# Kernel optimization log

Hardware: AMD Instinct MI355X
Metric: run time of the kernel (lower is better)

Reference implementation:

```python
import jax, jax.numpy as jnp
import numpy as np

EPS = 1e-8
E, H, F, MCL, V = 256, 512, 100, 500, 128000
CTX = MCL - 1  # encoder facts; decoder appends the mean-fact row
NUM_FACTS = 300


def setup_inputs() -> dict:
    key = jax.random.key(0)
    ks = jax.random.split(key, 16)

    def nrm(k, shape, s=0.02):
        return (jax.random.normal(k, shape) * s).astype(jnp.float32)

    return {
        "context": jax.random.randint(ks[0], (CTX, F), 0, V),
        "word_emb": nrm(ks[1], (V, E)),
        "attn1_W": nrm(ks[2], (MCL, E + H)),
        "attn1_b": nrm(ks[3], (MCL,)),
        "attn2_W": nrm(ks[4], (1, MCL)),
        "attn2_b": nrm(ks[5], (1,)),
        "W_ih": nrm(ks[6], (3 * H, 2 * E + F)),
        "W_hh": nrm(ks[7], (3 * H, H)),
        "b_ih": nrm(ks[8], (3 * H,)),
        "b_hh": nrm(ks[9], (3 * H,)),
        "out1_W": nrm(ks[10], (H, E + H)),
        "out1_b": nrm(ks[11], (H,)),
        "out2_W": nrm(ks[12], (V, H)),
        "out2_b": nrm(ks[13], (V,)),
        "h0": jnp.zeros((1, 1, H), jnp.float32),
        "num_facts": NUM_FACTS,
    }


def _encode(context, word_emb):
    # EncoderModule: embedding lookup + PositionalFactEncoder
    emb = word_emb[context]  # [CTX, F, E]
    s = jnp.arange(F, dtype=jnp.float32) / (F - 1)  # slen axis
    e = jnp.arange(E, dtype=jnp.float32) / (E - 1)  # elen axis
    l = 1.0 - s[:, None] - e[None, :] * (1.0 - 2.0 * s[:, None])  # [F, E]
    return jnp.sum(emb * l[None], axis=1)  # [CTX, E]


def reference(context, word_emb, attn1_W, attn1_b, attn2_W, attn2_b,
              W_ih, W_hh, b_ih, b_hh, out1_W, out1_b, out2_W, out2_b,
              h0, num_facts):
    facts = _encode(context, word_emb)  # [CTX, E]
    mean_fact = jnp.mean(facts[:num_facts], axis=0, keepdims=True)  # [1, E]
    fact_embeddings = jnp.concatenate([facts, mean_fact], axis=0)  # [MCL, E]

    # fact-level attention
    h = jnp.broadcast_to(h0.reshape(1, H), (MCL, H))
    attn_in = jnp.concatenate([fact_embeddings, h], axis=1)  # [MCL, E+H]
    e1 = jnp.tanh(attn_in @ attn1_W.T + attn1_b)  # [MCL, MCL]
    energy = (e1 @ attn2_W.T + attn2_b).reshape(1, -1)  # [1, MCL]
    aw = jax.nn.softmax(energy, axis=1)

    # mask: first num_facts ones, zeros, then 1 for the mean/generate slot
    idx = jnp.arange(MCL)
    mask = jnp.where((idx < num_facts) | (idx == MCL - 1), 1.0, 0.0)[None, :]
    aw = aw * mask + EPS
    aw = aw / jnp.sum(aw)
    log_aw = jnp.log(aw)  # [1, MCL]

    attn_weighted_facts = aw @ fact_embeddings  # [1, E]
    f_max_idx = jnp.argmax(aw, axis=1)[0]
    emb_f_max = fact_embeddings[f_max_idx].reshape(1, E)

    # decoder input: embedding of token 1 + zero positional input
    dec_word = word_emb[1].reshape(1, E)
    dec_pos = jnp.zeros((1, F), jnp.float32)
    x = jnp.concatenate([dec_word, dec_pos, emb_f_max], axis=1)  # [1, 2E+F]

    # torch GRU cell (gates ordered r, z, n)
    hprev = h0.reshape(1, H)
    gi = x @ W_ih.T + b_ih
    gh = hprev @ W_hh.T + b_hh
    r = jax.nn.sigmoid(gi[:, :H] + gh[:, :H])
    z = jax.nn.sigmoid(gi[:, H:2 * H] + gh[:, H:2 * H])
    n = jnp.tanh(gi[:, 2 * H:] + r * gh[:, 2 * H:])
    h_new = (1.0 - z) * n + z * hprev  # [1, H]

    # generate branch (f_t == max_context_len - 1): vocab head
    out = jnp.concatenate([h_new, attn_weighted_facts], axis=1)  # [1, H+E]
    out = jax.nn.relu(out @ out1_W.T + out1_b)
    logits = out @ out2_W.T + out2_b  # [1, V]
    y_pred = jax.nn.log_softmax(logits, axis=1)

    decoder_hidden = h_new.reshape(1, 1, H)
    return y_pred, log_aw, decoder_hidden
```

## Files before the change

### kernel.cpp

```cpp
#include <hip/hip_runtime.h>
#include <math.h>

#define E_    256
#define H_    512
#define F_    100
#define MCL_  500
#define CTX_  499
#define V_    128000
#define EPS_  1e-8f

typedef float f4v __attribute__((ext_vector_type(4)));

#define WS_FE      0
#define WS_ENERGY  (WS_FE + MCL_*E_)
#define WS_EBIAS   (WS_ENERGY + MCL_)
#define WS_AW      (WS_EBIAS + MCL_)
#define WS_AWFP    (WS_AW + 512)
#define WS_FMAX    (WS_AWFP + 8*E_)
#define WS_HNEW    (WS_FMAX + E_)
#define WS_ACT     (WS_HNEW + H_)
#define WS_LOGITS  (WS_ACT + H_)
#define WS_BSUM    (WS_LOGITS + V_)
#define WS_CNT     (WS_BSUM + 1024)

__device__ __forceinline__ float wred64(float v) {
#pragma unroll
  for (int o = 32; o; o >>= 1) v += __shfl_xor(v, o, 64);
  return v;
}
__device__ __forceinline__ float qred16(float v) {
#pragma unroll
  for (int o = 8; o; o >>= 1) v += __shfl_xor(v, o, 64);
  return v;
}
__device__ __forceinline__ float dot4(float4 a, float4 b) {
  return a.x*b.x + a.y*b.y + a.z*b.z + a.w*b.w;
}
__device__ __forceinline__ float dot4v(f4v a, f4v b) {
  return a.x*b.x + a.y*b.y + a.z*b.z + a.w*b.w;
}

__global__ __launch_bounds__(256) void k_encode(const int* __restrict__ ctx,
                                                const float* __restrict__ wemb,
                                                float* __restrict__ fe,
                                                const float* __restrict__ a1W,
                                                const float* __restrict__ a1b,
                                                const float* __restrict__ h0,
                                                float* __restrict__ ebias,
                                                int* __restrict__ cnt) {
  __shared__ int toks[2][F_];
  const int t = threadIdx.x;
  if (blockIdx.x >= 250) {
    const int lane = t & 63, sub = lane & 15, grp = lane >> 4;
    const int wid = (blockIdx.x - 250) * 4 + (t >> 6);
    const float4* h4 = (const float4*)h0;
    float4 hr[8];
#pragma unroll
    for (int q = 0; q < 8; ++q) hr[q] = h4[sub + q * 16];
    for (int j0 = wid * 4; j0 < MCL_; j0 += 32 * 4) {
      const int j = j0 + grp;
      if (j < MCL_) {
        const float4* w4 = (const float4*)(a1W + (size_t)j * (E_ + H_) + E_);
        float acc = 0.f;
#pragma unroll
        for (int q = 0; q < 8; ++q) acc += dot4(w4[sub + q * 16], hr[q]);
        acc = qred16(acc);
        if (sub == 0) ebias[j] = acc + a1b[j];
      }
    }
    return;
  }
  if (blockIdx.x == 0 && t == 0) *cnt = 0;
  const int i0 = blockIdx.x * 2;
  const int i1 = i0 + 1;
  if (t < F_) toks[0][t] = ctx[i0 * F_ + t];
  else if (t < 2 * F_) toks[1][t - F_] = (i1 < CTX_) ? ctx[i1 * F_ + (t - F_)] : 0;
  __syncthreads();
  const int row = t >> 7, tt = t & 127;
  const int i = i0 + row;
  const float e0n = (2 * tt) * (1.0f / 255.0f);
  const float e1n = (2 * tt + 1) * (1.0f / 255.0f);
  float ax = 0.f, ay = 0.f, bx = 0.f, by = 0.f;
#pragma unroll
  for (int f0 = 0; f0 < F_; f0 += 10) {
    float2 vb[10];
#pragma unroll
    for (int u = 0; u < 10; ++u)
      vb[u] = ((const float2*)(wemb + (size_t)toks[row][f0 + u] * E_))[tt];
#pragma unroll
    for (int u = 0; u < 10; ++u) {
      float s = (f0 + u) * (1.0f / 99.0f);
      float A = 1.0f - s, B = 1.0f - 2.0f * s;
      if (u & 1) { bx = fmaf(vb[u].x, A - e0n * B, bx); by = fmaf(vb[u].y, A - e1n * B, by); }
      else       { ax = fmaf(vb[u].x, A - e0n * B, ax); ay = fmaf(vb[u].y, A - e1n * B, ay); }
    }
  }
  if (i < CTX_) {
    float2 r; r.x = ax + bx; r.y = ay + by;
    ((float2*)(fe + (size_t)i * E_))[tt] = r;
  }
}

__global__ __launch_bounds__(256) void k_energy(float* __restrict__ fe,
                                                const float* __restrict__ a1W,
                                                const float* __restrict__ ebias,
                                                const float* __restrict__ a2W,
                                                const float* __restrict__ a2b,
                                                const int* __restrict__ nfp,
                                                float* __restrict__ energy,
                                                float* __restrict__ aw_ws,
                                                float* __restrict__ fmaxrow,
                                                float* __restrict__ out_logaw,
                                                int* __restrict__ cnt) {
  __shared__ float sfe[4][E_];
  __shared__ float sred[4][256];
  __shared__ int sticket;
  const int t = threadIdx.x;
  const int i0 = blockIdx.x * 4;
  const int nf = *nfp;

  if (blockIdx.x == 124) {
    float s0 = 0.f, s1 = 0.f, s2 = 0.f, s3 = 0.f;
    float s4 = 0.f, s5 = 0.f, s6 = 0.f, s7 = 0.f;
    int i = 0;
    for (; i + 8 <= nf; i += 8) {
      s0 += fe[(i + 0) * E_ + t]; s1 += fe[(i + 1) * E_ + t];
      s2 += fe[(i + 2) * E_ + t]; s3 += fe[(i + 3) * E_ + t];
      s4 += fe[(i + 4) * E_ + t]; s5 += fe[(i + 5) * E_ + t];
      s6 += fe[(i + 6) * E_ + t]; s7 += fe[(i + 7) * E_ + t];
    }
    for (; i < nf; ++i) s0 += fe[i * E_ + t];
    float mv = (((s0 + s1) + (s2 + s3)) + ((s4 + s5) + (s6 + s7))) / (float)nf;
    sfe[3][t] = mv;
    fe[CTX_ * E_ + t] = mv;
    sfe[0][t] = fe[496 * E_ + t];
    sfe[1][t] = fe[497 * E_ + t];
    sfe[2][t] = fe[498 * E_ + t];
  } else {
#pragma unroll
    for (int r = 0; r < 4; ++r) sfe[r][t] = fe[(i0 + r) * E_ + t];
  }
  __syncthreads();
  float c0 = 0.f, c1 = 0.f, c2 = 0.f, c3 = 0.f;
  const float4* s0p = (const float4*)sfe[0];
  const float4* s1p = (const float4*)sfe[1];
  const float4* s2p = (const float4*)sfe[2];
  const float4* s3p = (const float4*)sfe[3];
  for (int j = t; j < MCL_; j += 256) {
    const float4* w4 = (const float4*)(a1W + (size_t)j * (E_ + H_));
    float d0 = 0.f, d1 = 0.f, d2 = 0.f, d3 = 0.f;
#pragma unroll 8
    for (int q = 0; q < E_ / 4; ++q) {
      float4 a = w4[q];
      d0 += dot4(a, s0p[q]);
      d1 += dot4(a, s1p[q]);
      d2 += dot4(a, s2p[q]);
      d3 += dot4(a, s3p[q]);
    }
    float bj = ebias[j], wj = a2W[j];
    c0 = fmaf(wj, tanhf(d0 + bj), c0);
    c1 = fmaf(wj, tanhf(d1 + bj), c1);
    c2 = fmaf(wj, tanhf(d2 + bj), c2);
    c3 = fmaf(wj, tanhf(d3 + bj), c3);
  }
  sred[0][t] = c0; sred[1][t] = c1; sred[2][t] = c2; sred[3][t] = c3;
  __syncthreads();
  for (int s = 128; s; s >>= 1) {
    if (t < s) {
#pragma unroll
      for (int r = 0; r < 4; ++r) sred[r][t] += sred[r][t + s];
    }
    __syncthreads();
  }
  if (t < 4) energy[i0 + t] = sred[t][0] + a2b[0];

  __threadfence();
  if (t == 0) sticket = atomicAdd(cnt, 1);
  __syncthreads();
  if (sticket != 124) return;
  __threadfence();

  float* red = sred[0];
  int* idx = (int*)sred[1];
  float ev0 = energy[t];
  float ev1 = (t + 256 < MCL_) ? energy[t + 256] : -1e30f;
  red[t] = fmaxf(ev0, ev1); __syncthreads();
  for (int s = 128; s; s >>= 1) { if (t < s) red[t] = fmaxf(red[t], red[t + s]); __syncthreads(); }
  const float mx = red[0]; __syncthreads();

  float p0 = __expf(ev0 - mx);
  float p1 = (t + 256 < MCL_) ? __expf(ev1 - mx) : 0.f;
  red[t] = p0 + p1; __syncthreads();
  for (int s = 128; s; s >>= 1) { if (t < s) red[t] += red[t + s]; __syncthreads(); }
  const float S1 = red[0]; __syncthreads();

  float m0 = ((t < nf) || (t == MCL_ - 1)) ? 1.f : 0.f;
  float m1 = (((t + 256) < nf) || ((t + 256) == MCL_ - 1)) ? 1.f : 0.f;
  float a0 = p0 / S1 * m0 + EPS_;
  float a1 = (t + 256 < MCL_) ? (p1 / S1 * m1 + EPS_) : 0.f;
  red[t] = a0 + a1; __syncthreads();
  for (int s = 128; s; s >>= 1) { if (t < s) red[t] += red[t + s]; __syncthreads(); }
  const float S2 = red[0]; __syncthreads();

  a0 /= S2; a1 /= S2;
  out_logaw[t] = logf(a0);
  aw_ws[t] = a0;
  if (t + 256 < MCL_) { out_logaw[t + 256] = logf(a1); aw_ws[t + 256] = a1; }

  float bv; int bi;
  if ((t + 256 < MCL_) && (a1 > a0)) { bv = a1; bi = t + 256; } else { bv = a0; bi = t; }
  red[t] = bv; idx[t] = bi; __syncthreads();
  for (int s = 128; s; s >>= 1) {
    if (t < s) {
      float o = red[t + s]; int oi = idx[t + s];
      if (o > red[t] || (o == red[t] && oi < idx[t])) { red[t] = o; idx[t] = oi; }
    }
    __syncthreads();
  }
  const int fidx = idx[0]; __syncthreads();
  fmaxrow[t] = fe[fidx * E_ + t];
}

__global__ __launch_bounds__(256) void k_gates_gru(const float* __restrict__ Wih,
                                                   const float* __restrict__ bih,
                                                   const float* __restrict__ Whh,
                                                   const float* __restrict__ bhh,
                                                   const float* __restrict__ wemb,
                                                   const float* __restrict__ fmaxrow,
                                                   const float* __restrict__ h0,
                                                   const float* __restrict__ aw,
                                                   const float* __restrict__ fe,
                                                   float* __restrict__ awfp,
                                                   float* __restrict__ hnew,
                                                   float* __restrict__ out_hidden) {
  const int t = threadIdx.x;
  const int b = blockIdx.x;
  if (b >= 128) {
    const int m = b - 128;
    const int lo = m * 63;
    const int hi = min(MCL_, lo + 63);
    float pa = 0.f, pb = 0.f, pc = 0.f, pd = 0.f;
    int i = lo;
    for (; i + 4 <= hi; i += 4) {
      pa = fmaf(aw[i], fe[i * E_ + t], pa);
      pb = fmaf(aw[i + 1], fe[(i + 1) * E_ + t], pb);
      pc = fmaf(aw[i + 2], fe[(i + 2) * E_ + t], pc);
      pd = fmaf(aw[i + 3], fe[(i + 3) * E_ + t], pd);
    }
    for (; i < hi; ++i) pa = fmaf(aw[i], fe[i * E_ + t], pa);
    awfp[m * E_ + t] = (pa + pb) + (pc + pd);
    return;
  }
  const int lane = t & 63, w = t >> 6;
  const int h = b * 4 + w;
  const float4* xa4 = (const float4*)(wemb + E_);
  const float4* xb4 = (const float4*)fmaxrow;
  const float4* h4  = (const float4*)h0;
  float4 xav = xa4[lane], xbv = xb4[lane];
  float4 hva = h4[lane], hvb = h4[lane + 64];
  const float* rr = Wih + (size_t)h * (2 * E_ + F_);
  const float* rz = Wih + (size_t)(H_ + h) * (2 * E_ + F_);
  const float* rn = Wih + (size_t)(2 * H_ + h) * (2 * E_ + F_);
  float gir = dot4(((const float4*)rr)[lane], xav) + dot4(((const float4*)(rr + E_ + F_))[lane], xbv);
  float giz = dot4(((const float4*)rz)[lane], xav) + dot4(((const float4*)(rz + E_ + F_))[lane], xbv);
  float gin = dot4(((const float4*)rn)[lane], xav) + dot4(((const float4*)(rn + E_ + F_))[lane], xbv);
  const float4* wr = (const float4*)(Whh + (size_t)h * H_);
  const float4* wz = (const float4*)(Whh + (size_t)(H_ + h) * H_);
  const float4* wn = (const float4*)(Whh + (size_t)(2 * H_ + h) * H_);
  float ghr = dot4(wr[lane], hva) + dot4(wr[lane + 64], hvb);
  float ghz = dot4(wz[lane], hva) + dot4(wz[lane + 64], hvb);
  float ghn = dot4(wn[lane], hva) + dot4(wn[lane + 64], hvb);
  gir = wred64(gir); giz = wred64(giz); gin = wred64(gin);
  ghr = wred64(ghr); ghz = wred64(ghz); ghn = wred64(ghn);
  if (lane == 0) {
    float r = 1.f / (1.f + __expf(-(gir + bih[h] + ghr + bhh[h])));
    float z = 1.f / (1.f + __expf(-(giz + bih[H_ + h] + ghz + bhh[H_ + h])));
    float n = tanhf(gin + bih[2 * H_ + h] + r * (ghn + bhh[2 * H_ + h]));
    float hv = (1.f - z) * n + z * h0[h];
    hnew[h] = hv;
    out_hidden[h] = hv;
  }
}

__global__ __launch_bounds__(256) void k_out1(const float* __restrict__ o1W,
                                              const float* __restrict__ o1b,
                                              const float* __restrict__ hnew,
                                              const float* __restrict__ awfp,
                                              float* __restrict__ act) {
  __shared__ float cat[H_ + E_];
  const int t = threadIdx.x;
#pragma unroll
  for (int idx = t; idx < H_; idx += 256) cat[idx] = hnew[idx];
  {
    float s = 0.f;
#pragma unroll
    for (int q = 0; q < 8; ++q) s += awfp[q * E_ + t];
    cat[H_ + t] = s;
  }
  __syncthreads();
  const int lane = t & 63, w = t >> 6;
  const int r = blockIdx.x * 4 + w;
  const float4* c4 = (const float4*)cat;
  const float4* w4 = (const float4*)(o1W + (size_t)r * (H_ + E_));
  float acc = 0.f;
#pragma unroll
  for (int q = 0; q < 3; ++q) acc += dot4(w4[lane + 64 * q], c4[lane + 64 * q]);
  acc = wred64(acc);
  if (lane == 0) act[r] = fmaxf(acc + o1b[r], 0.f);
}

__global__ __launch_bounds__(256) void k_vocab(const float* __restrict__ o2W,
                                               const float* __restrict__ o2b,
                                               const float* __restrict__ act,
                                               float* __restrict__ logits,
                                               float* __restrict__ bsum) {
  __shared__ float swsum[4];
  const int t = threadIdx.x;
  const int lane = t & 63, sub = lane & 15, grp = lane >> 4, w = t >> 6;
  const int gw = blockIdx.x * 4 + w;
  const int nW = 1024 * 4;
  const f4v* a4 = (const f4v*)act;
  f4v ar[8];
#pragma unroll
  for (int q = 0; q < 8; ++q) ar[q] = a4[sub + q * 16];
  float sumexp = 0.f;
  for (int v0 = gw * 8; v0 < V_; v0 += nW * 8) {
    const int vA = v0 + grp;
    const int vB = v0 + 4 + grp;
    float accA = 0.f, accB = 0.f;
    if (vB < V_) {
      const f4v* wa = (const f4v*)(o2W + (size_t)vA * H_);
      const f4v* wb = (const f4v*)(o2W + (size_t)vB * H_);
      f4v la[8], lb[8];
#pragma unroll
      for (int q = 0; q < 8; ++q) la[q] = __builtin_nontemporal_load(&wa[sub + q * 16]);
#pragma unroll
      for (int q = 0; q < 8; ++q) lb[q] = __builtin_nontemporal_load(&wb[sub + q * 16]);
#pragma unroll
      for (int q = 0; q < 8; ++q) { accA += dot4v(la[q], ar[q]); accB += dot4v(lb[q], ar[q]); }
    } else if (vA < V_) {
      const f4v* wa = (const f4v*)(o2W + (size_t)vA * H_);
      f4v la[8];
#pragma unroll
      for (int q = 0; q < 8; ++q) la[q] = __builtin_nontemporal_load(&wa[sub + q * 16]);
#pragma unroll
      for (int q = 0; q < 8; ++q) accA += dot4v(la[q], ar[q]);
    }
    accA = qred16(accA);
    accB = qred16(accB);
    if (sub == 0) {
      if (vA < V_) { float lg = accA + o2b[vA]; logits[vA] = lg; sumexp += __expf(lg); }
      if (vB < V_) { float lg = accB + o2b[vB]; logits[vB] = lg; sumexp += __expf(lg); }
    }
  }
  sumexp = wred64(sumexp);
  if (lane == 0) swsum[w] = sumexp;
  __syncthreads();
  if (t == 0) bsum[blockIdx.x] = swsum[0] + swsum[1] + swsum[2] + swsum[3];
}

__global__ __launch_bounds__(256) void k_final(const float* __restrict__ logits,
                                               const float* __restrict__ bsum,
                                               float* __restrict__ y) {
  __shared__ float sr[256];
  const int t = threadIdx.x;
  float s = bsum[t] + bsum[t + 256] + bsum[t + 512] + bsum[t + 768];
  sr[t] = s; __syncthreads();
  for (int o = 128; o; o >>= 1) { if (t < o) sr[t] += sr[t + o]; __syncthreads(); }
  const float lz = logf(sr[0]);
  const int i = blockIdx.x * 256 + t;
  float4 l = ((const float4*)logits)[i];
  ((float4*)y)[i] = make_float4(l.x - lz, l.y - lz, l.z - lz, l.w - lz);
}

extern "C" void kernel_launch(void* const* d_in, const int* in_sizes, int n_in,
                              void* d_out, int out_size, void* d_ws, size_t ws_size,
                              hipStream_t stream) {
  const int*   ctx  = (const int*)d_in[0];
  const float* wemb = (const float*)d_in[1];
  const float* a1W  = (const float*)d_in[2];
  const float* a1b  = (const float*)d_in[3];
  const float* a2W  = (const float*)d_in[4];
  const float* a2b  = (const float*)d_in[5];
  const float* Wih  = (const float*)d_in[6];
  const float* Whh  = (const float*)d_in[7];
  const float* bih  = (const float*)d_in[8];
  const float* bhh  = (const float*)d_in[9];
  const float* o1W  = (const float*)d_in[10];
  const float* o1b  = (const float*)d_in[11];
  const float* o2W  = (const float*)d_in[12];
  const float* o2b  = (const float*)d_in[13];
  const float* h0   = (const float*)d_in[14];
  const int*   nfp  = (const int*)d_in[15];
  float* ws = (float*)d_ws;
  float* y  = (float*)d_out;
  int* cnt = (int*)(ws + WS_CNT);

  k_encode<<<258, 256, 0, stream>>>(ctx, wemb, ws + WS_FE, a1W, a1b, h0,
                                    ws + WS_EBIAS, cnt);
  k_energy<<<125, 256, 0, stream>>>(ws + WS_FE, a1W, ws + WS_EBIAS, a2W, a2b, nfp,
                                    ws + WS_ENERGY, ws + WS_AW, ws + WS_FMAX,
                                    y + V_, cnt);
  k_gates_gru<<<136, 256, 0, stream>>>(Wih, bih, Whh, bhh, wemb, ws + WS_FMAX, h0,
                                       ws + WS_AW, ws + WS_FE, ws + WS_AWFP,
                                       ws + WS_HNEW, y + V_ + MCL_);
  k_out1<<<128, 256, 0, stream>>>(o1W, o1b, ws + WS_HNEW, ws + WS_AWFP, ws + WS_ACT);
  k_vocab<<<1024, 256, 0, stream>>>(o2W, o2b, ws + WS_ACT, ws + WS_LOGITS, ws + WS_BSUM);
  k_final<<<V_ / 1024, 256, 0, stream>>>(ws + WS_LOGITS, ws + WS_BSUM, y);
}
```

Measured before the change: 120.2 us.

## Fuse out1, vocab and log-softmax into one persistent kernel with atomic grid sync

Merges the out1 projection, the vocab GEMV and the final log-softmax normalisation into a single 1000-block kernel. Atomic counters with spin-waits act as grid barriers: first for the 128 blocks producing the activation, then for the global sum-of-exp, which the last-arriving block reduces and publishes. Logits stay in registers and are written straight to the output, so the workspace logits round trip and two kernel launches go away. The spin barriers need all 1000 blocks to be co-resident (launch_bounds 256,4 is meant to allow this), otherwise the kernel can deadlock.

```diff
diff --git a/kernel.cpp b/kernel.cpp
--- a/kernel.cpp
+++ b/kernel.cpp
@@ -19,8 +19,7 @@
 #define WS_FMAX    (WS_AWFP + 8*E_)
 #define WS_HNEW    (WS_FMAX + E_)
 #define WS_ACT     (WS_HNEW + H_)
-#define WS_LOGITS  (WS_ACT + H_)
-#define WS_BSUM    (WS_LOGITS + V_)
+#define WS_BSUM    (WS_ACT + H_)
 #define WS_CNT     (WS_BSUM + 1024)
 
 __device__ __forceinline__ float wred64(float v) {
@@ -70,7 +69,7 @@
     }
     return;
   }
-  if (blockIdx.x == 0 && t == 0) *cnt = 0;
+  if (blockIdx.x == 0 && t < 4) cnt[t] = 0;
   const int i0 = blockIdx.x * 2;
   const int i1 = i0 + 1;
   if (t < F_) toks[0][t] = ctx[i0 * F_ + t];
@@ -282,95 +281,112 @@
   }
 }
 
-__global__ __launch_bounds__(256) void k_out1(const float* __restrict__ o1W,
-                                              const float* __restrict__ o1b,
-                                              const float* __restrict__ hnew,
-                                              const float* __restrict__ awfp,
-                                              float* __restrict__ act) {
-  __shared__ float cat[H_ + E_];
-  const int t = threadIdx.x;
-#pragma unroll
-  for (int idx = t; idx < H_; idx += 256) cat[idx] = hnew[idx];
-  {
-    float s = 0.f;
-#pragma unroll
-    for (int q = 0; q < 8; ++q) s += awfp[q * E_ + t];
-    cat[H_ + t] = s;
-  }
-  __syncthreads();
-  const int lane = t & 63, w = t >> 6;
-  const int r = blockIdx.x * 4 + w;
-  const float4* c4 = (const float4*)cat;
-  const float4* w4 = (const float4*)(o1W + (size_t)r * (H_ + E_));
-  float acc = 0.f;
-#pragma unroll
-  for (int q = 0; q < 3; ++q) acc += dot4(w4[lane + 64 * q], c4[lane + 64 * q]);
-  acc = wred64(acc);
-  if (lane == 0) act[r] = fmaxf(acc + o1b[r], 0.f);
-}
-
-__global__ __launch_bounds__(256) void k_vocab(const float* __restrict__ o2W,
-                                               const float* __restrict__ o2b,
-                                               const float* __restrict__ act,
-                                               float* __restrict__ logits,
-                                               float* __restrict__ bsum) {
+__global__ __launch_bounds__(256, 4) void k_mega(const float* __restrict__ o1W,
+                                                 const float* __restrict__ o1b,
+                                                 const float* __restrict__ hnew,
+                                                 const float* __restrict__ awfp,
+                                                 const float* __restrict__ o2W,
+                                                 const float* __restrict__ o2b,
+                                                 float* __restrict__ act,
+                                                 float* __restrict__ bsum,
+                                                 int* __restrict__ cnt,
+                                                 float* __restrict__ y) {
+  __shared__ float sact[H_];
+  __shared__ float sredf[256];
   __shared__ float swsum[4];
-  const int t = threadIdx.x;
+  __shared__ int ssh;
+  const int t = threadIdx.x, b = blockIdx.x;
   const int lane = t & 63, sub = lane & 15, grp = lane >> 4, w = t >> 6;
-  const int gw = blockIdx.x * 4 + w;
-  const int nW = 1024 * 4;
-  const f4v* a4 = (const f4v*)act;
+
+  if (b < 128) {
+    __shared__ float cat[H_ + E_];
+    for (int idx = t; idx < H_; idx += 256) cat[idx] = hnew[idx];
+    {
+      float s = 0.f;
+#pragma unroll
+      for (int q = 0; q < 8; ++q) s += awfp[q * E_ + t];
+      cat[H_ + t] = s;
+    }
+    __syncthreads();
+    const int r = b * 4 + w;
+    const float4* c4 = (const float4*)cat;
+    const float4* w4 = (const float4*)(o1W + (size_t)r * (H_ + E_));
+    float acc = 0.f;
+#pragma unroll
+    for (int q = 0; q < 3; ++q) acc += dot4(w4[lane + 64 * q], c4[lane + 64 * q]);
+    acc = wred64(acc);
+    if (lane == 0)
+      __hip_atomic_store(act + r, fmaxf(acc + o1b[r], 0.f),
+                         __ATOMIC_RELAXED, __HIP_MEMORY_SCOPE_AGENT);
+    __syncthreads();
+    if (t == 0)
+      __hip_atomic_fetch_add(cnt + 1, 1, __ATOMIC_RELEASE, __HIP_MEMORY_SCOPE_AGENT);
+  }
+
+  if (t == 0) {
+    while (__hip_atomic_load(cnt + 1, __ATOMIC_ACQUIRE, __HIP_MEMORY_SCOPE_AGENT) < 128)
+      __builtin_amdgcn_s_sleep(8);
+  }
+  __syncthreads();
+  for (int idx = t; idx < H_; idx += 256)
+    sact[idx] = __hip_atomic_load(act + idx, __ATOMIC_RELAXED, __HIP_MEMORY_SCOPE_AGENT);
+  __syncthreads();
+
+  const int gid = b * 4 + w;
   f4v ar[8];
 #pragma unroll
-  for (int q = 0; q < 8; ++q) ar[q] = a4[sub + q * 16];
+  for (int q = 0; q < 8; ++q) ar[q] = ((const f4v*)sact)[sub + q * 16];
+  float lg[8];
   float sumexp = 0.f;
-  for (int v0 = gw * 8; v0 < V_; v0 += nW * 8) {
-    const int vA = v0 + grp;
-    const int vB = v0 + 4 + grp;
-    float accA = 0.f, accB = 0.f;
-    if (vB < V_) {
-      const f4v* wa = (const f4v*)(o2W + (size_t)vA * H_);
-      const f4v* wb = (const f4v*)(o2W + (size_t)vB * H_);
-      f4v la[8], lb[8];
-#pragma unroll
-      for (int q = 0; q < 8; ++q) la[q] = __builtin_nontemporal_load(&wa[sub + q * 16]);
-#pragma unroll
-      for (int q = 0; q < 8; ++q) lb[q] = __builtin_nontemporal_load(&wb[sub + q * 16]);
-#pragma unroll
-      for (int q = 0; q < 8; ++q) { accA += dot4v(la[q], ar[q]); accB += dot4v(lb[q], ar[q]); }
-    } else if (vA < V_) {
-      const f4v* wa = (const f4v*)(o2W + (size_t)vA * H_);
-      f4v la[8];
-#pragma unroll
-      for (int q = 0; q < 8; ++q) la[q] = __builtin_nontemporal_load(&wa[sub + q * 16]);
-#pragma unroll
-      for (int q = 0; q < 8; ++q) accA += dot4v(la[q], ar[q]);
-    }
-    accA = qred16(accA);
-    accB = qred16(accB);
-    if (sub == 0) {
-      if (vA < V_) { float lg = accA + o2b[vA]; logits[vA] = lg; sumexp += __expf(lg); }
-      if (vB < V_) { float lg = accB + o2b[vB]; logits[vB] = lg; sumexp += __expf(lg); }
-    }
-  }
+#pragma unroll
+  for (int i = 0; i < 8; ++i) {
+    const int v = i * 16000 + gid * 4 + grp;
+    const f4v* wrow = (const f4v*)(o2W + (size_t)v * H_);
+    f4v la[8];
+#pragma unroll
+    for (int q = 0; q < 8; ++q) la[q] = __builtin_nontemporal_load(&wrow[sub + q * 16]);
+    float acc = 0.f;
+#pragma unroll
+    for (int q = 0; q < 8; ++q) acc += dot4v(la[q], ar[q]);
+    acc = qred16(acc);
+    float l = acc + o2b[v];
+    lg[i] = l;
+    if (sub == 0) sumexp += __expf(l);
+  }
+
   sumexp = wred64(sumexp);
   if (lane == 0) swsum[w] = sumexp;
   __syncthreads();
-  if (t == 0) bsum[blockIdx.x] = swsum[0] + swsum[1] + swsum[2] + swsum[3];
-}
-
-__global__ __launch_bounds__(256) void k_final(const float* __restrict__ logits,
-                                               const float* __restrict__ bsum,
-                                               float* __restrict__ y) {
-  __shared__ float sr[256];
-  const int t = threadIdx.x;
-  float s = bsum[t] + bsum[t + 256] + bsum[t + 512] + bsum[t + 768];
-  sr[t] = s; __syncthreads();
-  for (int o = 128; o; o >>= 1) { if (t < o) sr[t] += sr[t + o]; __syncthreads(); }
-  const float lz = logf(sr[0]);
-  const int i = blockIdx.x * 256 + t;
-  float4 l = ((const float4*)logits)[i];
-  ((float4*)y)[i] = make_float4(l.x - lz, l.y - lz, l.z - lz, l.w - lz);
+  if (t == 0) {
+    __hip_atomic_store(bsum + b, swsum[0] + swsum[1] + swsum[2] + swsum[3],
+                       __ATOMIC_RELAXED, __HIP_MEMORY_SCOPE_AGENT);
+    ssh = __hip_atomic_fetch_add(cnt + 2, 1, __ATOMIC_ACQ_REL, __HIP_MEMORY_SCOPE_AGENT);
+  }
+  __syncthreads();
+  if (ssh == 999) {
+    float s = 0.f;
+    for (int i = t; i < 1000; i += 256)
+      s += __hip_atomic_load(bsum + i, __ATOMIC_RELAXED, __HIP_MEMORY_SCOPE_AGENT);
+    sredf[t] = s; __syncthreads();
+    for (int o = 128; o; o >>= 1) { if (t < o) sredf[t] += sredf[t + o]; __syncthreads(); }
+    if (t == 0)
+      __hip_atomic_store(cnt + 3, __float_as_int(logf(sredf[0])),
+                         __ATOMIC_RELEASE, __HIP_MEMORY_SCOPE_AGENT);
+  }
+
+  if (t == 0) {
+    int f;
+    while ((f = __hip_atomic_load(cnt + 3, __ATOMIC_ACQUIRE, __HIP_MEMORY_SCOPE_AGENT)) == 0)
+      __builtin_amdgcn_s_sleep(8);
+    ssh = f;
+  }
+  __syncthreads();
+  const float lz = __int_as_float(ssh);
+  if (sub == 0) {
+#pragma unroll
+    for (int i = 0; i < 8; ++i)
+      y[i * 16000 + gid * 4 + grp] = lg[i] - lz;
+  }
 }
 
 extern "C" void kernel_launch(void* const* d_in, const int* in_sizes, int n_in,
@@ -404,7 +420,6 @@
   k_gates_gru<<<136, 256, 0, stream>>>(Wih, bih, Whh, bhh, wemb, ws + WS_FMAX, h0,
                                        ws + WS_AW, ws + WS_FE, ws + WS_AWFP,
                                        ws + WS_HNEW, y + V_ + MCL_);
-  k_out1<<<128, 256, 0, stream>>>(o1W, o1b, ws + WS_HNEW, ws + WS_AWFP, ws + WS_ACT);
-  k_vocab<<<1024, 256, 0, stream>>>(o2W, o2b, ws + WS_ACT, ws + WS_LOGITS, ws + WS_BSUM);
-  k_final<<<V_ / 1024, 256, 0, stream>>>(ws + WS_LOGITS, ws + WS_BSUM, y);
-}
+  k_mega<<<1000, 256, 0, stream>>>(o1W, o1b, ws + WS_HNEW, ws + WS_AWFP,
+                                   o2W, o2b, ws + WS_ACT, ws + WS_BSUM, cnt, y);
+}
```

Result: slower. 372.6 us (+210.0%).
